# Performance work log

Measured on AMD Instinct MI355X. Metric: run time of the kernel, lower is better.

Reference implementation:

```python
import jax, jax.numpy as jnp
import numpy as np

N_NODES = 50000
N_EDGES = 800000
D = 64
STEPS = 10
NEG_SLOPE = 0.2


def setup_inputs() -> dict:
    key = jax.random.key(0)
    ks = jax.random.split(key, 9)
    x = jax.random.normal(ks[0], (N_NODES, D), dtype=jnp.float32)
    edge_index_l1 = jax.random.randint(ks[1], (2, N_EDGES), 0, N_NODES, dtype=jnp.int64 if jax.config.jax_enable_x64 else jnp.int32)
    edge_index_l2 = jax.random.randint(ks[2], (2, N_EDGES), 0, N_NODES, dtype=jnp.int64 if jax.config.jax_enable_x64 else jnp.int32)
    s = 1.0 / np.sqrt(D)
    W1 = jax.random.normal(ks[3], (D, D), dtype=jnp.float32) * s
    a1_src = jax.random.normal(ks[4], (D,), dtype=jnp.float32) * s
    a1_dst = jax.random.normal(ks[5], (D,), dtype=jnp.float32) * s
    W2 = jax.random.normal(ks[6], (D, D), dtype=jnp.float32) * s
    a2_src = jax.random.normal(ks[7], (D,), dtype=jnp.float32) * s
    a2_dst = jax.random.normal(ks[8], (D,), dtype=jnp.float32) * s
    return {
        "x": x,
        "edge_index_l1": edge_index_l1,
        "edge_index_l2": edge_index_l2,
        "W1": W1, "a1_src": a1_src, "a1_dst": a1_dst,
        "W2": W2, "a2_src": a2_src, "a2_dst": a2_dst,
    }


def _gat_layer(x, src, dst, W, a_src, a_dst):
    """Single-head GATConv: out_i = sum_{j->i} softmax_i(LeakyReLU(a_s.Wx_j + a_d.Wx_i)) * Wx_j."""
    h = x @ W                                            # [N, D]
    e = jax.nn.leaky_relu((h @ a_src)[src] + (h @ a_dst)[dst], NEG_SLOPE)  # [E]
    # numerically stable segment softmax over incoming edges of each dst node
    m = jax.ops.segment_max(e, dst, num_segments=N_NODES)
    m = jax.lax.stop_gradient(jnp.where(jnp.isfinite(m), m, 0.0))
    w = jnp.exp(e - m[dst])                              # [E]
    denom = jax.ops.segment_sum(w, dst, num_segments=N_NODES)
    att = w / (denom[dst] + 1e-16)                       # [E]
    return jax.ops.segment_sum(h[src] * att[:, None], dst, num_segments=N_NODES)


def _base_operator(xt, ei1, ei2, W1, a1_src, a1_dst, W2, a2_src, a2_dst):
    h = _gat_layer(xt, ei1[0], ei1[1], W1, a1_src, a1_dst)
    h = jax.nn.elu(h)
    return _gat_layer(h, ei2[0], ei2[1], W2, a2_src, a2_dst)


def reference(x, edge_index_l1, edge_index_l2, W1, a1_src, a1_dst, W2, a2_src, a2_dst):
    ts = jnp.linspace(0.0, 1.0, STEPS, dtype=x.dtype)    # [STEPS]
    h_step = ts[1] - ts[0]                               # trapezoid-like uniform weight

    def step(acc, t):
        out = _base_operator(x * t, edge_index_l1, edge_index_l2,
                             W1, a1_src, a1_dst, W2, a2_src, a2_dst)
        return acc + out, None

    result, _ = jax.lax.scan(step, jnp.zeros_like(x), ts)
    return result * h_step
```

## Files before the change

### kernel.cpp

```cpp
#include <hip/hip_runtime.h>
#include <hip/hip_bf16.h>

#define NN 50000
#define NE 800000
#define DD 64
#define NEG 0.2f

#define RFL(x) __builtin_amdgcn_readfirstlane(x)
typedef unsigned short u16;

__global__ void k_hist(const int* __restrict__ dst1, const int* __restrict__ dst2,
                       int* __restrict__ cnt1, int* __restrict__ cnt2,
                       int* __restrict__ rank1, int* __restrict__ rank2) {
    int t = blockIdx.x * blockDim.x + threadIdx.x;
    if (t < NE / 4) {
        int4 d1 = ((const int4*)dst1)[t];
        int4 d2 = ((const int4*)dst2)[t];
        int4 r1, r2;
        r1.x = atomicAdd(&cnt1[d1.x], 1); r1.y = atomicAdd(&cnt1[d1.y], 1);
        r1.z = atomicAdd(&cnt1[d1.z], 1); r1.w = atomicAdd(&cnt1[d1.w], 1);
        r2.x = atomicAdd(&cnt2[d2.x], 1); r2.y = atomicAdd(&cnt2[d2.y], 1);
        r2.z = atomicAdd(&cnt2[d2.z], 1); r2.w = atomicAdd(&cnt2[d2.w], 1);
        ((int4*)rank1)[t] = r1;
        ((int4*)rank2)[t] = r2;
    }
}

__global__ __launch_bounds__(1024) void k_scan(const int* __restrict__ cnt1, int* __restrict__ off1,
                                               const int* __restrict__ cnt2, int* __restrict__ off2) {
    const int* cnt = blockIdx.x ? cnt2 : cnt1;
    int* off = blockIdx.x ? off2 : off1;
    __shared__ int lds[1024];
    const int tid = threadIdx.x;
    const int CH = (NN + 1023) / 1024;
    const int base = tid * CH;
    int s = 0;
    for (int q = 0; q < CH; ++q) {
        int idx = base + q;
        if (idx < NN) s += cnt[idx];
    }
    lds[tid] = s;
    __syncthreads();
    for (int d = 1; d < 1024; d <<= 1) {
        int v = (tid >= d) ? lds[tid - d] : 0;
        __syncthreads();
        lds[tid] += v;
        __syncthreads();
    }
    int run = tid ? lds[tid - 1] : 0;
    for (int q = 0; q < CH; ++q) {
        int idx = base + q;
        if (idx < NN) { off[idx] = run; run += cnt[idx]; }
    }
    if (tid == 1023) off[NN] = lds[1023];
}

__global__ void k_place(const int* __restrict__ src1, const int* __restrict__ dst1,
                        const int* __restrict__ off1, const int* __restrict__ rank1,
                        u16* __restrict__ csr1,
                        const int* __restrict__ src2, const int* __restrict__ dst2,
                        const int* __restrict__ off2, const int* __restrict__ rank2,
                        u16* __restrict__ csr2) {
    int t = blockIdx.x * blockDim.x + threadIdx.x;
    if (t < NE / 4) {
        int4 s1 = ((const int4*)src1)[t];
        int4 d1 = ((const int4*)dst1)[t];
        int4 r1 = ((const int4*)rank1)[t];
        int4 s2 = ((const int4*)src2)[t];
        int4 d2 = ((const int4*)dst2)[t];
        int4 r2 = ((const int4*)rank2)[t];
        csr1[off1[d1.x] + r1.x] = (u16)s1.x;
        csr1[off1[d1.y] + r1.y] = (u16)s1.y;
        csr1[off1[d1.z] + r1.z] = (u16)s1.z;
        csr1[off1[d1.w] + r1.w] = (u16)s1.w;
        csr2[off2[d2.x] + r2.x] = (u16)s2.x;
        csr2[off2[d2.y] + r2.y] = (u16)s2.y;
        csr2[off2[d2.z] + r2.z] = (u16)s2.z;
        csr2[off2[d2.w] + r2.w] = (u16)s2.w;
    }
}

__global__ __launch_bounds__(256) void k_h1(
    const float* __restrict__ x, const float* __restrict__ W1,
    const float* __restrict__ a1s, const float* __restrict__ a1d,
    _Float16* __restrict__ H1h, float* __restrict__ al1s, float* __restrict__ al1d) {
    const int lane = threadIdx.x & 63;
    const int i = blockIdx.x * 4 + (threadIdx.x >> 6);
    const float xv = x[i * DD + lane];
    float h = 0.f;
#pragma unroll
    for (int j = 0; j < DD; ++j) h = fmaf(__shfl(xv, j), W1[j * DD + lane], h);
    H1h[(size_t)i * DD + lane] = (_Float16)h;
    float ps = h * a1s[lane], pd = h * a1d[lane];
#pragma unroll
    for (int o = 32; o; o >>= 1) { ps += __shfl_xor(ps, o); pd += __shfl_xor(pd, o); }
    if (lane == 0) { al1s[i] = ps; al1d[i] = pd; }
}

__global__ void k_a2t(const float* __restrict__ W2, const float* __restrict__ a2s,
                      const float* __restrict__ a2d, float* __restrict__ t2s,
                      float* __restrict__ t2d) {
    int j = threadIdx.x & 63;
    float ss = 0.f, sd = 0.f;
#pragma unroll
    for (int d = 0; d < DD; ++d) {
        float w = W2[j * DD + d];
        ss = fmaf(w, a2s[d], ss);
        sd = fmaf(w, a2d[d], sd);
    }
    t2s[j] = ss;
    t2d[j] = sd;
}

__global__ __launch_bounds__(256) void k_l1(
    const int* __restrict__ off, const u16* __restrict__ csrc,
    const float* __restrict__ al1s, const float* __restrict__ al1d,
    const _Float16* __restrict__ H1h,
    const float* __restrict__ t2s, const float* __restrict__ t2d,
    uint4* __restrict__ H2a, _Float16* __restrict__ H2b,
    float* __restrict__ al2s8, float* __restrict__ al2s9, float* __restrict__ al2d) {
    __shared__ int2 lsr[4][64];
    const int lane = threadIdx.x & 63;
    const int wid = threadIdx.x >> 6;
    const int i = blockIdx.x * 4 + wid;
    const int p0 = RFL(off[i]);
    const int p1 = RFL(off[i + 1]);
    const float adv = al1d[i];
    float num[9], den[9];
#pragma unroll
    for (int k = 0; k < 9; ++k) { num[k] = 0.f; den[k] = 0.f; }

    for (int base = p0; base < p1; base += 64) {
        int m = p1 - base; if (m > 64) m = 64;
        int sv = 0; float rv = 0.f;
        if (lane < m) {
            sv = csrc[base + lane];
            float z = al1s[sv] + adv;
            float c = z > 0.f ? z : NEG * z;
            rv = __expf(c * (1.f / 9.f));
        }
        {
            float w = rv;
#pragma unroll
            for (int k = 0; k < 9; ++k) { den[k] += w; w *= rv; }
        }
        lsr[wid][lane] = make_int2(sv, __float_as_int(rv));
        asm volatile("s_waitcnt lgkmcnt(0)" ::: "memory");
        int j = 0;
        for (; j + 3 < m; j += 4) {
            int2 e0 = lsr[wid][j], e1 = lsr[wid][j + 1];
            int2 e2 = lsr[wid][j + 2], e3 = lsr[wid][j + 3];
            float h0 = (float)H1h[(size_t)e0.x * DD + lane];
            float h1v = (float)H1h[(size_t)e1.x * DD + lane];
            float h2v = (float)H1h[(size_t)e2.x * DD + lane];
            float h3v = (float)H1h[(size_t)e3.x * DD + lane];
            float r0 = __int_as_float(e0.y), r1 = __int_as_float(e1.y);
            float r2 = __int_as_float(e2.y), r3 = __int_as_float(e3.y);
            float w0 = r0, w1 = r1, w2 = r2, w3 = r3;
#pragma unroll
            for (int k = 0; k < 9; ++k) {
                num[k] = fmaf(w0, h0, num[k]);  w0 *= r0;
                num[k] = fmaf(w1, h1v, num[k]); w1 *= r1;
                num[k] = fmaf(w2, h2v, num[k]); w2 *= r2;
                num[k] = fmaf(w3, h3v, num[k]); w3 *= r3;
            }
        }
        for (; j < m; ++j) {
            int2 e0 = lsr[wid][j];
            float h0 = (float)H1h[(size_t)e0.x * DD + lane];
            float r0 = __int_as_float(e0.y);
            float w0 = r0;
#pragma unroll
            for (int k = 0; k < 9; ++k) { num[k] = fmaf(w0, h0, num[k]); w0 *= r0; }
        }
    }
#pragma unroll
    for (int k = 0; k < 9; ++k) {
#pragma unroll
        for (int o = 32; o; o >>= 1) den[k] += __shfl_xor(den[k], o);
    }

    const float tss = t2s[lane];
    const float tdd = t2d[lane];
    float hm[9];
#pragma unroll
    for (int k = 0; k < 9; ++k) {
        float t = (float)(k + 1) * (1.f / 9.f);
        float v = (den[k] > 0.f) ? (t * num[k] / den[k]) : 0.f;
        hm[k] = (v > 0.f) ? v : expm1f(v);
    }
#pragma unroll
    for (int k = 0; k < 9; ++k) {
        float ps = hm[k] * tss, pd = hm[k] * tdd;
#pragma unroll
        for (int o = 32; o; o >>= 1) { ps += __shfl_xor(ps, o); pd += __shfl_xor(pd, o); }
        if (lane == 0) {
            if (k < 8) al2s8[(size_t)i * 8 + k] = ps;
            else       al2s9[i] = ps;
            al2d[(size_t)i * 9 + k] = pd;
        }
    }
    union { _Float16 h[8]; uint4 u; } pk;
#pragma unroll
    for (int k = 0; k < 8; ++k) pk.h[k] = (_Float16)hm[k];
    H2a[(size_t)i * DD + lane] = pk.u;
    H2b[(size_t)i * DD + lane] = (_Float16)hm[8];
}

__global__ __launch_bounds__(256) void k_l2(
    const int* __restrict__ off, const u16* __restrict__ csrc,
    const float* __restrict__ al2s8, const float* __restrict__ al2s9,
    const float* __restrict__ al2d,
    const uint4* __restrict__ H2a, const _Float16* __restrict__ H2b,
    const float* __restrict__ W2, float* __restrict__ out) {
    __shared__ float lw[4][64][12];
    const int lane = threadIdx.x & 63;
    const int wid = threadIdx.x >> 6;
    const int i = blockIdx.x * 4 + wid;
    const int p0 = RFL(off[i]);
    const int p1 = RFL(off[i + 1]);
    float adv[9];
#pragma unroll
    for (int k = 0; k < 9; ++k) adv[k] = al2d[(size_t)i * 9 + k];
    float num[9], den[9];
#pragma unroll
    for (int k = 0; k < 9; ++k) { num[k] = 0.f; den[k] = 0.f; }

    for (int base = p0; base < p1; base += 64) {
        int m = p1 - base; if (m > 64) m = 64;
        int sv = 0; float wv[9];
#pragma unroll
        for (int k = 0; k < 9; ++k) wv[k] = 0.f;
        if (lane < m) {
            sv = csrc[base + lane];
            const float4* pa = (const float4*)(al2s8 + (size_t)sv * 8);
            float4 A0 = pa[0], A1 = pa[1];
            float as[9] = {A0.x, A0.y, A0.z, A0.w, A1.x, A1.y, A1.z, A1.w, al2s9[sv]};
#pragma unroll
            for (int k = 0; k < 9; ++k) {
                float z = as[k] + adv[k];
                float lr = z > 0.f ? z : NEG * z;
                wv[k] = __expf(lr);
            }
        }
#pragma unroll
        for (int k = 0; k < 9; ++k) den[k] += wv[k];
        float* dst = &lw[wid][lane][0];
        *(float4*)dst       = make_float4(wv[0], wv[1], wv[2], wv[3]);
        *(float4*)(dst + 4) = make_float4(wv[4], wv[5], wv[6], wv[7]);
        dst[8] = wv[8];
        dst[9] = __int_as_float(sv);
        asm volatile("s_waitcnt lgkmcnt(0)" ::: "memory");
        int j = 0;
        for (; j + 1 < m; j += 2) {
            const float* s0 = &lw[wid][j][0];
            const float* s1 = &lw[wid][j + 1][0];
            int sj0 = __float_as_int(s0[9]);
            int sj1 = __float_as_int(s1[9]);
            union { uint4 v; _Float16 h[8]; } c0, c1;
            c0.v = H2a[(size_t)sj0 * DD + lane];
            c1.v = H2a[(size_t)sj1 * DD + lane];
            float h90 = (float)H2b[(size_t)sj0 * DD + lane];
            float h91 = (float)H2b[(size_t)sj1 * DD + lane];
            float4 wA0 = *(const float4*)s0, wB0 = *(const float4*)(s0 + 4);
            float4 wA1 = *(const float4*)s1, wB1 = *(const float4*)(s1 + 4);
            num[0] = fmaf(wA0.x, (float)c0.h[0], num[0]);
            num[1] = fmaf(wA0.y, (float)c0.h[1], num[1]);
            num[2] = fmaf(wA0.z, (float)c0.h[2], num[2]);
            num[3] = fmaf(wA0.w, (float)c0.h[3], num[3]);
            num[4] = fmaf(wB0.x, (float)c0.h[4], num[4]);
            num[5] = fmaf(wB0.y, (float)c0.h[5], num[5]);
            num[6] = fmaf(wB0.z, (float)c0.h[6], num[6]);
            num[7] = fmaf(wB0.w, (float)c0.h[7], num[7]);
            num[8] = fmaf(s0[8], h90, num[8]);
            num[0] = fmaf(wA1.x, (float)c1.h[0], num[0]);
            num[1] = fmaf(wA1.y, (float)c1.h[1], num[1]);
            num[2] = fmaf(wA1.z, (float)c1.h[2], num[2]);
            num[3] = fmaf(wA1.w, (float)c1.h[3], num[3]);
            num[4] = fmaf(wB1.x, (float)c1.h[4], num[4]);
            num[5] = fmaf(wB1.y, (float)c1.h[5], num[5]);
            num[6] = fmaf(wB1.z, (float)c1.h[6], num[6]);
            num[7] = fmaf(wB1.w, (float)c1.h[7], num[7]);
            num[8] = fmaf(s1[8], h91, num[8]);
        }
        if (j < m) {
            const float* s0 = &lw[wid][j][0];
            int sj0 = __float_as_int(s0[9]);
            union { uint4 v; _Float16 h[8]; } c0;
            c0.v = H2a[(size_t)sj0 * DD + lane];
            float h90 = (float)H2b[(size_t)sj0 * DD + lane];
            float4 wA0 = *(const float4*)s0, wB0 = *(const float4*)(s0 + 4);
            num[0] = fmaf(wA0.x, (float)c0.h[0], num[0]);
            num[1] = fmaf(wA0.y, (float)c0.h[1], num[1]);
            num[2] = fmaf(wA0.z, (float)c0.h[2], num[2]);
            num[3] = fmaf(wA0.w, (float)c0.h[3], num[3]);
            num[4] = fmaf(wB0.x, (float)c0.h[4], num[4]);
            num[5] = fmaf(wB0.y, (float)c0.h[5], num[5]);
            num[6] = fmaf(wB0.z, (float)c0.h[6], num[6]);
            num[7] = fmaf(wB0.w, (float)c0.h[7], num[7]);
            num[8] = fmaf(s0[8], h90, num[8]);
        }
    }
#pragma unroll
    for (int k = 0; k < 9; ++k) {
#pragma unroll
        for (int o = 32; o; o >>= 1) den[k] += __shfl_xor(den[k], o);
    }
    float vsum = 0.f;
#pragma unroll
    for (int k = 0; k < 9; ++k) vsum += (den[k] > 0.f) ? (num[k] / den[k]) : 0.f;
    float h2 = 0.f;
#pragma unroll 8
    for (int j = 0; j < DD; ++j) h2 = fmaf(__shfl(vsum, j), W2[j * DD + lane], h2);
    out[(size_t)i * DD + lane] = h2 * (1.f / 9.f);
}

extern "C" void kernel_launch(void* const* d_in, const int* in_sizes, int n_in,
                              void* d_out, int out_size, void* d_ws, size_t ws_size,
                              hipStream_t stream) {
    const float* x   = (const float*)d_in[0];
    const int*   ei1 = (const int*)d_in[1];
    const int*   ei2 = (const int*)d_in[2];
    const float* W1  = (const float*)d_in[3];
    const float* a1s = (const float*)d_in[4];
    const float* a1d = (const float*)d_in[5];
    const float* W2  = (const float*)d_in[6];
    const float* a2s = (const float*)d_in[7];
    const float* a2d = (const float*)d_in[8];
    float* out = (float*)d_out;

    const int* src1 = ei1;
    const int* dst1 = ei1 + NE;
    const int* src2 = ei2;
    const int* dst2 = ei2 + NE;

    uint4* H2a    = (uint4*)d_ws;
    _Float16* H1h = (_Float16*)((float*)d_ws + (size_t)NN * 256);
    float* al1s   = (float*)H1h + (size_t)NN * DD / 2;
    float* al1d   = al1s + NN;
    float* al2s8  = al1d + NN;
    float* al2s9  = al2s8 + (size_t)NN * 8;
    float* al2d   = al2s9 + NN;
    _Float16* H2b = (_Float16*)(al2d + (size_t)NN * 9);
    int* rank1 = (int*)((float*)H2b + (size_t)NN * DD / 2);
    int* rank2 = rank1 + NE;
    u16* csr1  = (u16*)(rank2 + NE);
    u16* csr2  = csr1 + NE;
    float* t2s = (float*)(csr2 + NE);
    float* t2d = t2s + DD;
    int* off1 = (int*)(t2d + DD);
    int* off2 = off1 + (NN + 1);
    int* cnt1 = off2 + (NN + 1);
    int* cnt2 = cnt1 + NN;

    const int EB = 256;
    const int EG4 = (NE / 4 + EB - 1) / EB;
    const int NB = NN / 4;

    hipMemsetAsync(cnt1, 0, 2 * NN * sizeof(int), stream);
    k_hist<<<EG4, EB, 0, stream>>>(dst1, dst2, cnt1, cnt2, rank1, rank2);
    k_scan<<<2, 1024, 0, stream>>>(cnt1, off1, cnt2, off2);
    k_place<<<EG4, EB, 0, stream>>>(src1, dst1, off1, rank1, csr1,
                                    src2, dst2, off2, rank2, csr2);
    k_h1<<<NB, 256, 0, stream>>>(x, W1, a1s, a1d, H1h, al1s, al1d);
    k_a2t<<<1, 64, 0, stream>>>(W2, a2s, a2d, t2s, t2d);

    k_l1<<<NB, 256, 0, stream>>>(off1, csr1, al1s, al1d, H1h,
                                 t2s, t2d, H2a, H2b, al2s8, al2s9, al2d);
    k_l2<<<NB, 256, 0, stream>>>(off2, csr2, al2s8, al2s9, al2d, H2a, H2b, W2, out);
}
```

Baseline: 473.9 us.

## Merge independent setup kernels into block-partitioned fat kernels to cut launches

Combines the histogram, node projection and W2·a precompute into one launch, with each block range doing a different job. Splits CSR placement so layer-2 placement runs inside the layer-1 aggregation kernel, and only layer-1 placement runs before it. This reduces the number of kernel launches and serial dependency points, and lets independent work overlap on the GPU. The cost is more register and LDS pressure from the fat kernels, which could lower occupancy for the aggregation blocks.

```diff
diff --git a/kernel.cpp b/kernel.cpp
--- a/kernel.cpp
+++ b/kernel.cpp
@@ -5,24 +5,60 @@
 #define NE 800000
 #define DD 64
 #define NEG 0.2f
+#define NB (NN / 4)
+#define EG4B ((NE / 4 + 255) / 256)
 
 #define RFL(x) __builtin_amdgcn_readfirstlane(x)
 typedef unsigned short u16;
 
-__global__ void k_hist(const int* __restrict__ dst1, const int* __restrict__ dst2,
-                       int* __restrict__ cnt1, int* __restrict__ cnt2,
-                       int* __restrict__ rank1, int* __restrict__ rank2) {
-    int t = blockIdx.x * blockDim.x + threadIdx.x;
-    if (t < NE / 4) {
-        int4 d1 = ((const int4*)dst1)[t];
-        int4 d2 = ((const int4*)dst2)[t];
-        int4 r1, r2;
-        r1.x = atomicAdd(&cnt1[d1.x], 1); r1.y = atomicAdd(&cnt1[d1.y], 1);
-        r1.z = atomicAdd(&cnt1[d1.z], 1); r1.w = atomicAdd(&cnt1[d1.w], 1);
-        r2.x = atomicAdd(&cnt2[d2.x], 1); r2.y = atomicAdd(&cnt2[d2.y], 1);
-        r2.z = atomicAdd(&cnt2[d2.z], 1); r2.w = atomicAdd(&cnt2[d2.w], 1);
-        ((int4*)rank1)[t] = r1;
-        ((int4*)rank2)[t] = r2;
+__global__ __launch_bounds__(256) void k_fat1(
+    const int* __restrict__ dst1, const int* __restrict__ dst2,
+    int* __restrict__ cnt1, int* __restrict__ cnt2,
+    int* __restrict__ rank1, int* __restrict__ rank2,
+    const float* __restrict__ x, const float* __restrict__ W1,
+    const float* __restrict__ a1s, const float* __restrict__ a1d,
+    _Float16* __restrict__ H1h, float* __restrict__ al1s, float* __restrict__ al1d,
+    const float* __restrict__ W2, const float* __restrict__ a2s,
+    const float* __restrict__ a2d, float* __restrict__ t2s, float* __restrict__ t2d) {
+    const int bid = blockIdx.x;
+    if (bid < EG4B) {
+        int t = bid * 256 + threadIdx.x;
+        if (t < NE / 4) {
+            int4 d1 = ((const int4*)dst1)[t];
+            int4 d2 = ((const int4*)dst2)[t];
+            int4 r1, r2;
+            r1.x = atomicAdd(&cnt1[d1.x], 1); r1.y = atomicAdd(&cnt1[d1.y], 1);
+            r1.z = atomicAdd(&cnt1[d1.z], 1); r1.w = atomicAdd(&cnt1[d1.w], 1);
+            r2.x = atomicAdd(&cnt2[d2.x], 1); r2.y = atomicAdd(&cnt2[d2.y], 1);
+            r2.z = atomicAdd(&cnt2[d2.z], 1); r2.w = atomicAdd(&cnt2[d2.w], 1);
+            ((int4*)rank1)[t] = r1;
+            ((int4*)rank2)[t] = r2;
+        }
+    } else if (bid < EG4B + NB) {
+        const int lane = threadIdx.x & 63;
+        const int i = (bid - EG4B) * 4 + (threadIdx.x >> 6);
+        const float xv = x[i * DD + lane];
+        float h = 0.f;
+#pragma unroll
+        for (int j = 0; j < DD; ++j) h = fmaf(__shfl(xv, j), W1[j * DD + lane], h);
+        H1h[(size_t)i * DD + lane] = (_Float16)h;
+        float ps = h * a1s[lane], pd = h * a1d[lane];
+#pragma unroll
+        for (int o = 32; o; o >>= 1) { ps += __shfl_xor(ps, o); pd += __shfl_xor(pd, o); }
+        if (lane == 0) { al1s[i] = ps; al1d[i] = pd; }
+    } else {
+        if (threadIdx.x < DD) {
+            int j = threadIdx.x;
+            float ss = 0.f, sd = 0.f;
+#pragma unroll
+            for (int d = 0; d < DD; ++d) {
+                float w = W2[j * DD + d];
+                ss = fmaf(w, a2s[d], ss);
+                sd = fmaf(w, a2d[d], sd);
+            }
+            t2s[j] = ss;
+            t2d[j] = sd;
+        }
     }
 }
 
@@ -55,64 +91,31 @@
     if (tid == 1023) off[NN] = lds[1023];
 }
 
-__global__ void k_place(const int* __restrict__ src1, const int* __restrict__ dst1,
-                        const int* __restrict__ off1, const int* __restrict__ rank1,
-                        u16* __restrict__ csr1,
-                        const int* __restrict__ src2, const int* __restrict__ dst2,
-                        const int* __restrict__ off2, const int* __restrict__ rank2,
-                        u16* __restrict__ csr2) {
-    int t = blockIdx.x * blockDim.x + threadIdx.x;
+__device__ __forceinline__ void place_body(int t, const int* __restrict__ src,
+                                           const int* __restrict__ dst,
+                                           const int* __restrict__ off,
+                                           const int* __restrict__ rank,
+                                           u16* __restrict__ csr) {
     if (t < NE / 4) {
-        int4 s1 = ((const int4*)src1)[t];
-        int4 d1 = ((const int4*)dst1)[t];
-        int4 r1 = ((const int4*)rank1)[t];
-        int4 s2 = ((const int4*)src2)[t];
-        int4 d2 = ((const int4*)dst2)[t];
-        int4 r2 = ((const int4*)rank2)[t];
-        csr1[off1[d1.x] + r1.x] = (u16)s1.x;
-        csr1[off1[d1.y] + r1.y] = (u16)s1.y;
-        csr1[off1[d1.z] + r1.z] = (u16)s1.z;
-        csr1[off1[d1.w] + r1.w] = (u16)s1.w;
-        csr2[off2[d2.x] + r2.x] = (u16)s2.x;
-        csr2[off2[d2.y] + r2.y] = (u16)s2.y;
-        csr2[off2[d2.z] + r2.z] = (u16)s2.z;
-        csr2[off2[d2.w] + r2.w] = (u16)s2.w;
-    }
-}
-
-__global__ __launch_bounds__(256) void k_h1(
-    const float* __restrict__ x, const float* __restrict__ W1,
-    const float* __restrict__ a1s, const float* __restrict__ a1d,
-    _Float16* __restrict__ H1h, float* __restrict__ al1s, float* __restrict__ al1d) {
-    const int lane = threadIdx.x & 63;
-    const int i = blockIdx.x * 4 + (threadIdx.x >> 6);
-    const float xv = x[i * DD + lane];
-    float h = 0.f;
-#pragma unroll
-    for (int j = 0; j < DD; ++j) h = fmaf(__shfl(xv, j), W1[j * DD + lane], h);
-    H1h[(size_t)i * DD + lane] = (_Float16)h;
-    float ps = h * a1s[lane], pd = h * a1d[lane];
-#pragma unroll
-    for (int o = 32; o; o >>= 1) { ps += __shfl_xor(ps, o); pd += __shfl_xor(pd, o); }
-    if (lane == 0) { al1s[i] = ps; al1d[i] = pd; }
-}
-
-__global__ void k_a2t(const float* __restrict__ W2, const float* __restrict__ a2s,
-                      const float* __restrict__ a2d, float* __restrict__ t2s,
-                      float* __restrict__ t2d) {
-    int j = threadIdx.x & 63;
-    float ss = 0.f, sd = 0.f;
-#pragma unroll
-    for (int d = 0; d < DD; ++d) {
-        float w = W2[j * DD + d];
-        ss = fmaf(w, a2s[d], ss);
-        sd = fmaf(w, a2d[d], sd);
-    }
-    t2s[j] = ss;
-    t2d[j] = sd;
-}
-
-__global__ __launch_bounds__(256) void k_l1(
+        int4 s = ((const int4*)src)[t];
+        int4 d = ((const int4*)dst)[t];
+        int4 r = ((const int4*)rank)[t];
+        csr[off[d.x] + r.x] = (u16)s.x;
+        csr[off[d.y] + r.y] = (u16)s.y;
+        csr[off[d.z] + r.z] = (u16)s.z;
+        csr[off[d.w] + r.w] = (u16)s.w;
+    }
+}
+
+__global__ void k_place1(const int* __restrict__ src, const int* __restrict__ dst,
+                         const int* __restrict__ off, const int* __restrict__ rank,
+                         u16* __restrict__ csr) {
+    place_body(blockIdx.x * blockDim.x + threadIdx.x, src, dst, off, rank, csr);
+}
+
+__global__ __launch_bounds__(256) void k_fat2(
+    const int* __restrict__ src2, const int* __restrict__ dst2,
+    const int* __restrict__ off2, const int* __restrict__ rank2, u16* __restrict__ csr2,
     const int* __restrict__ off, const u16* __restrict__ csrc,
     const float* __restrict__ al1s, const float* __restrict__ al1d,
     const _Float16* __restrict__ H1h,
@@ -120,9 +123,14 @@
     uint4* __restrict__ H2a, _Float16* __restrict__ H2b,
     float* __restrict__ al2s8, float* __restrict__ al2s9, float* __restrict__ al2d) {
     __shared__ int2 lsr[4][64];
+    const int bid = blockIdx.x;
+    if (bid < EG4B) {
+        place_body(bid * 256 + threadIdx.x, src2, dst2, off2, rank2, csr2);
+        return;
+    }
     const int lane = threadIdx.x & 63;
     const int wid = threadIdx.x >> 6;
-    const int i = blockIdx.x * 4 + wid;
+    const int i = (bid - EG4B) * 4 + wid;
     const int p0 = RFL(off[i]);
     const int p1 = RFL(off[i + 1]);
     const float adv = al1d[i];
@@ -353,19 +361,16 @@
     int* cnt1 = off2 + (NN + 1);
     int* cnt2 = cnt1 + NN;
 
-    const int EB = 256;
-    const int EG4 = (NE / 4 + EB - 1) / EB;
-    const int NB = NN / 4;
-
     hipMemsetAsync(cnt1, 0, 2 * NN * sizeof(int), stream);
-    k_hist<<<EG4, EB, 0, stream>>>(dst1, dst2, cnt1, cnt2, rank1, rank2);
+    k_fat1<<<EG4B + NB + 1, 256, 0, stream>>>(
+        dst1, dst2, cnt1, cnt2, rank1, rank2,
+        x, W1, a1s, a1d, H1h, al1s, al1d,
+        W2, a2s, a2d, t2s, t2d);
     k_scan<<<2, 1024, 0, stream>>>(cnt1, off1, cnt2, off2);
-    k_place<<<EG4, EB, 0, stream>>>(src1, dst1, off1, rank1, csr1,
-                                    src2, dst2, off2, rank2, csr2);
-    k_h1<<<NB, 256, 0, stream>>>(x, W1, a1s, a1d, H1h, al1s, al1d);
-    k_a2t<<<1, 64, 0, stream>>>(W2, a2s, a2d, t2s, t2d);
-
-    k_l1<<<NB, 256, 0, stream>>>(off1, csr1, al1s, al1d, H1h,
-                                 t2s, t2d, H2a, H2b, al2s8, al2s9, al2d);
+    k_place1<<<EG4B, 256, 0, stream>>>(src1, dst1, off1, rank1, csr1);
+    k_fat2<<<EG4B + NB, 256, 0, stream>>>(
+        src2, dst2, off2, rank2, csr2,
+        off1, csr1, al1s, al1d, H1h, t2s, t2d,
+        H2a, H2b, al2s8, al2s9, al2d);
     k_l2<<<NB, 256, 0, stream>>>(off2, csr2, al2s8, al2s9, al2d, H2a, H2b, W2, out);
 }
```

New measurement: 458.3 us (median of 2 runs). 3.3% less time.
